# Kernel optimization log

Hardware: AMD Instinct MI355X
Metric: run time of the kernel (lower is better)

Reference implementation:

```python
import jax, jax.numpy as jnp
import numpy as np

N, H, O, E = 32768, 512, 512, 16


def setup_inputs() -> dict:
    key = jax.random.key(0)
    k0, k1, k2 = jax.random.split(key, 3)
    x = jax.random.normal(k0, (N, H), dtype=jnp.float32)
    # gate Linear(H -> E)
    Wg = jax.random.normal(k1, (E, H), dtype=jnp.float32) * (1.0 / np.sqrt(H))
    bg = jnp.zeros((E,), dtype=jnp.float32)
    # expert Linears(H -> O), stacked [E, O, H]
    We = jax.random.normal(k2, (E, O, H), dtype=jnp.float32) * (1.0 / np.sqrt(H))
    be = jnp.zeros((E, O), dtype=jnp.float32)
    return {"x": x, "Wg": Wg, "bg": bg, "We": We, "be": be}


def reference(x, Wg, bg, We, be):
    # gate: softmax over experts, then top-1 (argmax)
    logits = x @ Wg.T + bg                       # [N, E]
    weights = jax.nn.softmax(logits, axis=-1)
    expert_idx = jnp.argmax(weights, axis=-1)    # [N]
    # run every expert on every token, then select the top-1 expert's output.
    # (note: original module does NOT scale output by the gate weight)
    all_out = jnp.einsum('nh,eoh->neo', x, We) + be[None]   # [N, E, O]
    out = jnp.take_along_axis(all_out, expert_idx[:, None, None], axis=1)[:, 0]  # [N, O]
    return out
```

## Files before the change

kernel.cpp:

```cpp
#include <hip/hip_runtime.h>
#include <hip/hip_bf16.h>
#include <stdint.h>

#define NTOK 32768
#define HDIM 512
#define ODIM 512
#define NEXP 16

#define TM 64
#define TN 128
#define BK 32
#define MTILES 64

#define CSTRIDE 32

#define GATE_BLKS (NTOK / 16)
#define CVT_BLKS (NEXP * ODIM * HDIM / 8 / 256)

typedef __bf16 bf16x8 __attribute__((ext_vector_type(8)));
typedef float  floatx4 __attribute__((ext_vector_type(4)));

__device__ __forceinline__ unsigned pk2(unsigned lo, unsigned hi) {
  return (lo >> 16) | (hi & 0xffff0000u);
}

__device__ __forceinline__ bf16x8 asbf8(uint4 u) { bf16x8 v; __builtin_memcpy(&v, &u, 16); return v; }

__device__ __forceinline__ void split3(float4 a, float4 b, uint4* H, uint4* M, uint4* L) {
  float f[8] = {a.x, a.y, a.z, a.w, b.x, b.y, b.z, b.w};
  unsigned h[8], m[8], l[8];
#pragma unroll
  for (int j = 0; j < 8; ++j) {
    union { float F; unsigned U; } u; u.F = f[j];
    h[j] = u.U & 0xffff0000u;
    union { unsigned U; float F; } hv; hv.U = h[j];
    float r1 = f[j] - hv.F;
    union { float F; unsigned U; } r1u; r1u.F = r1;
    m[j] = r1u.U & 0xffff0000u;
    union { unsigned U; float F; } mv; mv.U = m[j];
    float r2 = r1 - mv.F;
    union { float F; unsigned U; } r2u; r2u.F = r2;
    l[j] = r2u.U;
  }
  H->x = pk2(h[0], h[1]); H->y = pk2(h[2], h[3]); H->z = pk2(h[4], h[5]); H->w = pk2(h[6], h[7]);
  M->x = pk2(m[0], m[1]); M->y = pk2(m[2], m[3]); M->z = pk2(m[4], m[5]); M->w = pk2(m[6], m[7]);
  L->x = pk2(l[0], l[1]); L->y = pk2(l[2], l[3]); L->z = pk2(l[4], l[5]); L->w = pk2(l[6], l[7]);
}

#define GLDS16(g, l) __builtin_amdgcn_global_load_lds( \
    (const __attribute__((address_space(1))) unsigned int*)(g), \
    (__attribute__((address_space(3))) unsigned int*)(l), 16, 0, 0)

__global__ __launch_bounds__(256, 4) void fused_prep(const float* __restrict__ x,
                                                     const float* __restrict__ Wg,
                                                     const float* __restrict__ bg,
                                                     const float* __restrict__ We,
                                                     int* __restrict__ counts,
                                                     int* __restrict__ buckets,
                                                     unsigned short* __restrict__ xbf,
                                                     unsigned short* __restrict__ webf) {
  __shared__ __align__(16) float red[4][16][20];

  int bid = blockIdx.x;
  int t = threadIdx.x;

  if (bid >= GATE_BLKS) {
    int i = (bid - GATE_BLKS) * 256 + t;
    const float4* src = (const float4*)We;
    float4 a = src[2 * i];
    float4 b = src[2 * i + 1];
    union { float F; unsigned U; } u[8] = {{a.x},{a.y},{a.z},{a.w},{b.x},{b.y},{b.z},{b.w}};
    uint4 o;
    o.x = pk2(u[0].U, u[1].U); o.y = pk2(u[2].U, u[3].U);
    o.z = pk2(u[4].U, u[5].U); o.w = pk2(u[6].U, u[7].U);
    ((uint4*)webf)[i] = o;
    return;
  }

  int lane = t & 63;
  int w = t >> 6;
  int tok0 = bid * 16;
  int fr = lane & 15;
  int quad = lane >> 4;

  const float* xb0 = x + (size_t)(tok0 + fr) * HDIM + w * 128 + quad * 8;
  const float* wg0 = Wg + (size_t)fr * HDIM + w * 128 + quad * 8;

  floatx4 acc = {};

  float4 xa = *(const float4*)(xb0);
  float4 xv = *(const float4*)(xb0 + 4);

#pragma unroll
  for (int si = 0; si < 4; ++si) {
    int s = w * 4 + si;
    float4 wa = *(const float4*)(wg0 + si * 32);
    float4 wb = *(const float4*)(wg0 + si * 32 + 4);
    uint4 BH, BM, BL;
    split3(wa, wb, &BH, &BM, &BL);
    bf16x8 bh = asbf8(BH), bm = asbf8(BM), bl = asbf8(BL);

    float4 nxa, nxv;
    if (si < 3) {
      nxa = *(const float4*)(xb0 + (si + 1) * 32);
      nxv = *(const float4*)(xb0 + (si + 1) * 32 + 4);
    }

    uint4 H, M, L;
    split3(xa, xv, &H, &M, &L);
    *(uint4*)(xbf + (size_t)(tok0 + fr) * HDIM + s * 32 + quad * 8) = H;
    bf16x8 ah = asbf8(H), am = asbf8(M), al = asbf8(L);
    acc = __builtin_amdgcn_mfma_f32_16x16x32_bf16(ah, bh, acc, 0, 0, 0);
    acc = __builtin_amdgcn_mfma_f32_16x16x32_bf16(ah, bm, acc, 0, 0, 0);
    acc = __builtin_amdgcn_mfma_f32_16x16x32_bf16(am, bh, acc, 0, 0, 0);
    acc = __builtin_amdgcn_mfma_f32_16x16x32_bf16(am, bm, acc, 0, 0, 0);
    acc = __builtin_amdgcn_mfma_f32_16x16x32_bf16(ah, bl, acc, 0, 0, 0);
    acc = __builtin_amdgcn_mfma_f32_16x16x32_bf16(al, bh, acc, 0, 0, 0);
    acc = __builtin_amdgcn_mfma_f32_16x16x32_bf16(am, bl, acc, 0, 0, 0);
    acc = __builtin_amdgcn_mfma_f32_16x16x32_bf16(al, bm, acc, 0, 0, 0);

    if (si < 3) { xa = nxa; xv = nxv; }
  }

#pragma unroll
  for (int i = 0; i < 4; ++i)
    red[w][quad * 4 + i][fr] = acc[i];
  __syncthreads();

  if (t < 16) {
    int r = t;
    float4 tot4[4];
#pragma unroll
    for (int eq = 0; eq < 4; ++eq) tot4[eq] = *(const float4*)&bg[eq * 4];
#pragma unroll
    for (int ww = 0; ww < 4; ++ww)
#pragma unroll
      for (int eq = 0; eq < 4; ++eq) {
        float4 v = *(const float4*)&red[ww][r][eq * 4];
        tot4[eq].x += v.x; tot4[eq].y += v.y; tot4[eq].z += v.z; tot4[eq].w += v.w;
      }
    float tot[16];
#pragma unroll
    for (int eq = 0; eq < 4; ++eq) {
      tot[eq * 4 + 0] = tot4[eq].x; tot[eq * 4 + 1] = tot4[eq].y;
      tot[eq * 4 + 2] = tot4[eq].z; tot[eq * 4 + 3] = tot4[eq].w;
    }
    float bv = tot[0]; int bi = 0;
#pragma unroll
    for (int e = 1; e < NEXP; ++e) if (tot[e] > bv) { bv = tot[e]; bi = e; }

    int token = tok0 + r;
    for (int ee = 0; ee < NEXP; ++ee) {
      int e = (ee + bid) & 15;
      unsigned long long mask = __ballot(bi == e);
      if (mask) {
        int leader = __builtin_ctzll(mask);
        int base = 0;
        if (lane == leader) base = atomicAdd(&counts[e << 5], (int)__popcll(mask));
        base = __shfl(base, leader, 64);
        if (bi == e) {
          int rank = (int)__popcll(mask & ((1ull << lane) - 1ull));
          buckets[e * NTOK + base + rank] = token;
        }
      }
    }
  }
}

__global__ __launch_bounds__(256, 6) void moe_gemm(const unsigned short* __restrict__ xbf,
                                                   const unsigned short* __restrict__ webf,
                                                   const float* __restrict__ be,
                                                   const int* __restrict__ counts,
                                                   const int* __restrict__ buckets,
                                                   float* __restrict__ out) {
  int lin = blockIdx.x;
  int swz = (lin & 7) * 512 + (lin >> 3);
  int e = swz >> 8;
  int rem = swz & 255;
  int o0 = (rem >> 6) * TN;
  int m0 = (rem & 63) * TM;

  int cnt = counts[e << 5];
  if (m0 >= cnt) return;

  __shared__ __align__(16) unsigned short As[2][TM * BK];
  __shared__ __align__(16) unsigned short Bs[2][TN * BK];
  __shared__ int toks[TM];

  int t = threadIdx.x;
  int lane = t & 63;
  int w = t >> 6;

  if (t < TM) {
    int r = m0 + t;
    toks[t] = (r < cnt) ? buckets[e * NTOK + r] : buckets[e * NTOK];
  }
  __syncthreads();

  int pl = lane >> 3;
  int sl = lane & 7;
  int slog = sl ^ pl;
  int rsub = 2 * pl + (slog >> 2);
  int cch = slog & 3;

  const unsigned short* agp = xbf + (size_t)toks[w * 16 + rsub] * HDIM + cch * 8;
  const unsigned short* bgp[2];
#pragma unroll
  for (int j = 0; j < 2; ++j) {
    int row = w * 32 + j * 16 + rsub;
    bgp[j] = webf + ((size_t)e * ODIM + o0 + row) * HDIM + cch * 8;
  }

  int wm = (w & 1) * 32;
  int wn = (w >> 1) * 64;
  int fr = lane & 15;
  int quad = lane >> 4;

  int aoff[2], boff[4];
#pragma unroll
  for (int mt = 0; mt < 2; ++mt) {
    int m = wm + mt * 16 + fr;
    int pr = m >> 1;
    aoff[mt] = pr * 64 + (((((m & 1) << 2) | quad) ^ (pr & 7)) << 3);
  }
#pragma unroll
  for (int nt = 0; nt < 4; ++nt) {
    int n = wn + nt * 16 + fr;
    int pn = n >> 1;
    boff[nt] = pn * 64 + (((((n & 1) << 2) | quad) ^ (pn & 7)) << 3);
  }

  float bias[4];
#pragma unroll
  for (int nt = 0; nt < 4; ++nt)
    bias[nt] = be[e * ODIM + o0 + wn + nt * 16 + fr];

  floatx4 acc[2][4] = {};

  GLDS16(agp, As[0] + w * 512);
#pragma unroll
  for (int j = 0; j < 2; ++j)
    GLDS16(bgp[j], Bs[0] + w * 1024 + j * 512);

  for (int k = 0; k < HDIM / BK; ++k) {
    int p = k & 1;
    asm volatile("s_waitcnt vmcnt(0)" ::: "memory");
    __syncthreads();
    if (k < HDIM / BK - 1) {
      int koff = (k + 1) * BK;
      GLDS16(agp + koff, As[1 - p] + w * 512);
#pragma unroll
      for (int j = 0; j < 2; ++j)
        GLDS16(bgp[j] + koff, Bs[1 - p] + w * 1024 + j * 512);
    }

    bf16x8 af[2], bfr[4];
#pragma unroll
    for (int mt = 0; mt < 2; ++mt)
      af[mt] = *(const bf16x8*)(As[p] + aoff[mt]);
#pragma unroll
    for (int nt = 0; nt < 4; ++nt)
      bfr[nt] = *(const bf16x8*)(Bs[p] + boff[nt]);
#pragma unroll
    for (int mt = 0; mt < 2; ++mt)
#pragma unroll
      for (int nt = 0; nt < 4; ++nt)
        acc[mt][nt] = __builtin_amdgcn_mfma_f32_16x16x32_bf16(af[mt], bfr[nt], acc[mt][nt], 0, 0, 0);
  }

  int rbase = wm + quad * 4;
#pragma unroll
  for (int nt = 0; nt < 4; ++nt) {
    int col = o0 + wn + nt * 16 + fr;
#pragma unroll
    for (int mt = 0; mt < 2; ++mt) {
#pragma unroll
      for (int i = 0; i < 4; ++i) {
        int rl = rbase + mt * 16 + i;
        if (m0 + rl < cnt) {
          out[(size_t)toks[rl] * ODIM + col] = acc[mt][nt][i] + bias[nt];
        }
      }
    }
  }
}

#define WS_BUCKETS 4096
#define WS_XBF (WS_BUCKETS + NEXP * NTOK * 4)
#define WS_WEBF (WS_XBF + NTOK * HDIM * 2)

extern "C" void kernel_launch(void* const* d_in, const int* in_sizes, int n_in,
                              void* d_out, int out_size, void* d_ws, size_t ws_size,
                              hipStream_t stream) {
  const float* x  = (const float*)d_in[0];
  const float* Wg = (const float*)d_in[1];
  const float* bg = (const float*)d_in[2];
  const float* We = (const float*)d_in[3];
  const float* be = (const float*)d_in[4];
  float* out = (float*)d_out;
  char* ws = (char*)d_ws;

  int* counts = (int*)ws;
  int* buckets = (int*)(ws + WS_BUCKETS);
  unsigned short* xbf  = (unsigned short*)(ws + WS_XBF);
  unsigned short* webf = (unsigned short*)(ws + WS_WEBF);

  (void)hipMemsetAsync(counts, 0, NEXP * CSTRIDE * 4, stream);
  fused_prep<<<GATE_BLKS + CVT_BLKS, 256, 0, stream>>>(x, Wg, bg, We, counts, buckets, xbf, webf);
  moe_gemm<<<MTILES * (ODIM / TN) * NEXP, 256, 0, stream>>>(xbf, webf, be, counts, buckets, out);
}
```

Baseline: 186.9 us.

## Load GEMM operands directly from global into registers, dropping LDS staging

Removes the LDS double buffer fed by global_load_lds in the MoE GEMM. Each wave now loads its MFMA fragments straight from global memory into registers, with register double-buffering across the fully unrolled K loop. This eliminates the per-step barriers and the LDS traffic. The cost is that data is no longer shared between waves, so each A and B row is fetched by multiple waves and global/L2 traffic goes up. Occupancy hint drops from 6 to 4 blocks to make room for the extra registers.

```diff
diff --git a/kernel.cpp b/kernel.cpp
--- a/kernel.cpp
+++ b/kernel.cpp
@@ -9,7 +9,6 @@
 
 #define TM 64
 #define TN 128
-#define BK 32
 #define MTILES 64
 
 #define CSTRIDE 32
@@ -46,10 +45,6 @@
   M->x = pk2(m[0], m[1]); M->y = pk2(m[2], m[3]); M->z = pk2(m[4], m[5]); M->w = pk2(m[6], m[7]);
   L->x = pk2(l[0], l[1]); L->y = pk2(l[2], l[3]); L->z = pk2(l[4], l[5]); L->w = pk2(l[6], l[7]);
 }
-
-#define GLDS16(g, l) __builtin_amdgcn_global_load_lds( \
-    (const __attribute__((address_space(1))) unsigned int*)(g), \
-    (__attribute__((address_space(3))) unsigned int*)(l), 16, 0, 0)
 
 __global__ __launch_bounds__(256, 4) void fused_prep(const float* __restrict__ x,
                                                      const float* __restrict__ Wg,
@@ -167,7 +162,7 @@
   }
 }
 
-__global__ __launch_bounds__(256, 6) void moe_gemm(const unsigned short* __restrict__ xbf,
+__global__ __launch_bounds__(256, 4) void moe_gemm(const unsigned short* __restrict__ xbf,
                                                    const unsigned short* __restrict__ webf,
                                                    const float* __restrict__ be,
                                                    const int* __restrict__ counts,
@@ -183,8 +178,6 @@
   int cnt = counts[e << 5];
   if (m0 >= cnt) return;
 
-  __shared__ __align__(16) unsigned short As[2][TM * BK];
-  __shared__ __align__(16) unsigned short Bs[2][TN * BK];
   __shared__ int toks[TM];
 
   int t = threadIdx.x;
@@ -196,39 +189,20 @@
     toks[t] = (r < cnt) ? buckets[e * NTOK + r] : buckets[e * NTOK];
   }
   __syncthreads();
-
-  int pl = lane >> 3;
-  int sl = lane & 7;
-  int slog = sl ^ pl;
-  int rsub = 2 * pl + (slog >> 2);
-  int cch = slog & 3;
-
-  const unsigned short* agp = xbf + (size_t)toks[w * 16 + rsub] * HDIM + cch * 8;
-  const unsigned short* bgp[2];
-#pragma unroll
-  for (int j = 0; j < 2; ++j) {
-    int row = w * 32 + j * 16 + rsub;
-    bgp[j] = webf + ((size_t)e * ODIM + o0 + row) * HDIM + cch * 8;
-  }
 
   int wm = (w & 1) * 32;
   int wn = (w >> 1) * 64;
   int fr = lane & 15;
   int quad = lane >> 4;
 
-  int aoff[2], boff[4];
-#pragma unroll
-  for (int mt = 0; mt < 2; ++mt) {
-    int m = wm + mt * 16 + fr;
-    int pr = m >> 1;
-    aoff[mt] = pr * 64 + (((((m & 1) << 2) | quad) ^ (pr & 7)) << 3);
-  }
-#pragma unroll
-  for (int nt = 0; nt < 4; ++nt) {
-    int n = wn + nt * 16 + fr;
-    int pn = n >> 1;
-    boff[nt] = pn * 64 + (((((n & 1) << 2) | quad) ^ (pn & 7)) << 3);
-  }
+  const unsigned short* ap[2];
+#pragma unroll
+  for (int mt = 0; mt < 2; ++mt)
+    ap[mt] = xbf + (size_t)toks[wm + mt * 16 + fr] * HDIM + quad * 8;
+  const unsigned short* bp[4];
+#pragma unroll
+  for (int nt = 0; nt < 4; ++nt)
+    bp[nt] = webf + ((size_t)e * ODIM + o0 + wn + nt * 16 + fr) * HDIM + quad * 8;
 
   float bias[4];
 #pragma unroll
@@ -237,35 +211,29 @@
 
   floatx4 acc[2][4] = {};
 
-  GLDS16(agp, As[0] + w * 512);
-#pragma unroll
-  for (int j = 0; j < 2; ++j)
-    GLDS16(bgp[j], Bs[0] + w * 1024 + j * 512);
-
-  for (int k = 0; k < HDIM / BK; ++k) {
-    int p = k & 1;
-    asm volatile("s_waitcnt vmcnt(0)" ::: "memory");
-    __syncthreads();
-    if (k < HDIM / BK - 1) {
-      int koff = (k + 1) * BK;
-      GLDS16(agp + koff, As[1 - p] + w * 512);
-#pragma unroll
-      for (int j = 0; j < 2; ++j)
-        GLDS16(bgp[j] + koff, Bs[1 - p] + w * 1024 + j * 512);
-    }
-
-    bf16x8 af[2], bfr[4];
+  bf16x8 af[2][2], bf[2][4];
+#pragma unroll
+  for (int mt = 0; mt < 2; ++mt) af[0][mt] = *(const bf16x8*)(ap[mt]);
+#pragma unroll
+  for (int nt = 0; nt < 4; ++nt) bf[0][nt] = *(const bf16x8*)(bp[nt]);
+
+#pragma unroll
+  for (int s = 0; s < HDIM / 32; ++s) {
+    int cur = s & 1;
+    int nxt = cur ^ 1;
+    if (s < HDIM / 32 - 1) {
+      int koff = (s + 1) * 32;
+#pragma unroll
+      for (int mt = 0; mt < 2; ++mt) af[nxt][mt] = *(const bf16x8*)(ap[mt] + koff);
+#pragma unroll
+      for (int nt = 0; nt < 4; ++nt) bf[nxt][nt] = *(const bf16x8*)(bp[nt] + koff);
+    }
 #pragma unroll
     for (int mt = 0; mt < 2; ++mt)
-      af[mt] = *(const bf16x8*)(As[p] + aoff[mt]);
-#pragma unroll
-    for (int nt = 0; nt < 4; ++nt)
-      bfr[nt] = *(const bf16x8*)(Bs[p] + boff[nt]);
-#pragma unroll
-    for (int mt = 0; mt < 2; ++mt)
 #pragma unroll
       for (int nt = 0; nt < 4; ++nt)
-        acc[mt][nt] = __builtin_amdgcn_mfma_f32_16x16x32_bf16(af[mt], bfr[nt], acc[mt][nt], 0, 0, 0);
+        acc[mt][nt] = __builtin_amdgcn_mfma_f32_16x16x32_bf16(af[cur][mt], bf[cur][nt],
+                                                              acc[mt][nt], 0, 0, 0);
   }
 
   int rbase = wm + quad * 4;
```

After: 256.5 us. 1.37x slower.
